# Performance work log

Measured on AMD Instinct MI355X. Metric: run time of the kernel, lower is better.

Reference implementation:

```python
import jax, jax.numpy as jnp
import numpy as np

NUM_EMB = 1024
EMB_DIM = 256
BETA = 0.25


def setup_inputs() -> dict:
    key = jax.random.key(0)
    k1, k2 = jax.random.split(key)
    z_e = jax.random.normal(k1, (32, EMB_DIM, 32, 32), dtype=jnp.float32)
    # original inits uniform(-1/num_emb, 1/num_emb)
    emb_weight = jax.random.uniform(k2, (NUM_EMB, EMB_DIM), dtype=jnp.float32,
                                    minval=-1.0 / NUM_EMB, maxval=1.0 / NUM_EMB)
    return {"z_e": z_e, "emb_weight": emb_weight}


def reference(z_e, emb_weight):
    # (B, C, H, W) -> (B, H, W, C)
    z = jnp.transpose(z_e, (0, 2, 3, 1))
    B, H, W, C = z.shape
    z_flat = z.reshape(-1, C)  # (N, C)
    # squared L2 distances to codebook: ||z||^2 + ||e||^2 - 2 z e^T
    d = (jnp.sum(z_flat ** 2, axis=1, keepdims=True)
         + jnp.sum(emb_weight ** 2, axis=1)
         - 2.0 * jnp.matmul(z_flat, emb_weight.T))  # (N, num_emb)
    encoding_indices = jnp.argmin(d, axis=1)  # (N,)
    # one-hot matmul == gather of codebook rows
    z_q = jnp.take(emb_weight, encoding_indices, axis=0).reshape(B, H, W, C)
    # vq losses
    L_e = jnp.mean((jax.lax.stop_gradient(z_q) - z) ** 2)
    L_q = jnp.mean((z_q - jax.lax.stop_gradient(z)) ** 2)
    vq_loss = L_e + BETA * L_q
    # straight-through estimator
    z_q_st = z + jax.lax.stop_gradient(z_q - z)
    z_q_out = jnp.transpose(z_q_st, (0, 3, 1, 2))  # (B, C, H, W)
    return z_q_out, vq_loss, encoding_indices
```

## Files before the change

### kernel.cpp

```cpp
#include <hip/hip_runtime.h>

#define NUM_EMB 1024
#define EMB_DIM 256
#define NPIX    32768
#define HW      1024
#define ZQ_ELEMS 8388608

#define WS_TNORM 8
#define WS_SNORM 8192
#define WS_KEYS  139264
#define WS_CNT   401408
#define WS_EPL   401424
#define EPLANE_ELEMS (NUM_EMB * EMB_DIM)

typedef unsigned long long u64;
typedef unsigned int u32;
typedef unsigned short u16;

typedef __bf16 bf16x8 __attribute__((ext_vector_type(8)));
typedef float f32x16 __attribute__((ext_vector_type(16)));
typedef u16 u16x8 __attribute__((ext_vector_type(8)));

#define ZIDX(row, q) (((row) << 5) + ((((q) ^ ((row) & 3))) << 3))

__device__ __forceinline__ float pw128_sq(const float* x, int stride) {
  float r[8];
#pragma unroll
  for (int j = 0; j < 8; ++j) {
    float v = x[(size_t)j * stride];
    r[j] = __fmul_rn(v, v);
  }
  for (int i = 8; i < 128; i += 8) {
#pragma unroll
    for (int j = 0; j < 8; ++j) {
      float v = x[(size_t)(i + j) * stride];
      r[j] = __fadd_rn(r[j], __fmul_rn(v, v));
    }
  }
  float s01 = __fadd_rn(r[0], r[1]);
  float s23 = __fadd_rn(r[2], r[3]);
  float s45 = __fadd_rn(r[4], r[5]);
  float s67 = __fadd_rn(r[6], r[7]);
  return __fadd_rn(__fadd_rn(s01, s23), __fadd_rn(s45, s67));
}

__device__ __forceinline__ void split3(float x, u16& h, u16& m, u16& l) {
  u32 u = __float_as_uint(x);
  u16 hb = (u16)((u + 0x7fffu + ((u >> 16) & 1u)) >> 16);
  float hf = __uint_as_float((u32)hb << 16);
  float r1 = x - hf;
  u32 u1 = __float_as_uint(r1);
  u16 mb = (u16)((u1 + 0x7fffu + ((u1 >> 16) & 1u)) >> 16);
  float mf = __uint_as_float((u32)mb << 16);
  float r2 = r1 - mf;
  u32 u2 = __float_as_uint(r2);
  u16 lb = (u16)((u2 + 0x7fffu + ((u2 >> 16) & 1u)) >> 16);
  h = hb; m = mb; l = lb;
}

__device__ __forceinline__ u64 shfl_xor_u64(u64 v, int msk) {
  const u32 lo = __shfl_xor((u32)v, msk, 64);
  const u32 hi = __shfl_xor((u32)(v >> 32), msk, 64);
  return ((u64)hi << 32) | lo;
}

__global__ __launch_bounds__(256) void vq_prep_kernel(
    const float* __restrict__ z, const float* __restrict__ emb,
    float* __restrict__ tnorm, float* __restrict__ snorm,
    unsigned long long* __restrict__ keys, double* __restrict__ loss_accum,
    u32* __restrict__ counter,
    u16* __restrict__ eh, u16* __restrict__ em, u16* __restrict__ el) {
  const int gid = blockIdx.x * 256 + threadIdx.x;
  if (gid == 0) *loss_accum = 0.0;
  if (gid == 1) *counter = 0u;
  if (gid < NPIX) {
    keys[gid] = ~0ull;
    const int b = gid >> 10, hw = gid & 1023;
    const float* base = z + (size_t)b * (EMB_DIM * HW) + hw;
    snorm[gid] = __fadd_rn(pw128_sq(base, HW), pw128_sq(base + (size_t)128 * HW, HW));
  } else {
    const int k = gid - NPIX;
    if (k < NUM_EMB) {
      const float* row = emb + (size_t)k * EMB_DIM;
      tnorm[k] = __fadd_rn(pw128_sq(row, 1), pw128_sq(row + 128, 1));
      for (int c = 0; c < EMB_DIM; c += 8) {
        u16x8 vh, vm, vl;
#pragma unroll
        for (int j = 0; j < 8; ++j) {
          u16 h_, m_, l_;
          split3(row[c + j], h_, m_, l_);
          vh[j] = h_; vm[j] = m_; vl[j] = l_;
        }
        *(u16x8*)(eh + (size_t)k * EMB_DIM + c) = vh;
        *(u16x8*)(em + (size_t)k * EMB_DIM + c) = vm;
        *(u16x8*)(el + (size_t)k * EMB_DIM + c) = vl;
      }
    }
  }
}

__global__ __launch_bounds__(256, 3) void vq_main_kernel(
    const float* __restrict__ z,
    const u16* __restrict__ eh, const u16* __restrict__ em,
    const u16* __restrict__ el,
    const float* __restrict__ tnorm, const float* __restrict__ snorm,
    unsigned long long* __restrict__ keys) {
  __shared__ __align__(16) u16 zs[3][4096];
  __shared__ __align__(16) u16 es[3][4096];

  const int t   = threadIdx.x;
  const int hb  = blockIdx.x;
  const int bid = (hb & 7) * 256 + (hb >> 3);
  const int pt  = bid >> 3;
  const int ntb = bid & 7;
  const int m0  = pt * 128;
  const int n0  = ntb * 128;
  const int b   = m0 >> 10;
  const int hw0 = m0 & 1023;
  const float* zbase = z + (size_t)b * (EMB_DIM * HW) + hw0;

  const int l    = t & 63;
  const int wid  = t >> 6;
  const int wpx0 = (wid >> 1) * 64;
  const int wcb  = (wid & 1) * 64;
  const int cl   = l & 31;
  const int hi   = l >> 5;

  const int sr  = t & 127;
  const int skh = (t >> 7) * 16;
  const int q0  = (t >> 7) * 2;

  const u16* eplan[3] = {eh, em, el};
  const size_t ebase = (size_t)(n0 + sr) * EMB_DIM + skh;

  float gz[16];
  u16x8 ge[3][2];

#pragma unroll
  for (int j = 0; j < 16; ++j)
    gz[j] = zbase[(size_t)(skh + j) * HW + sr];
#pragma unroll
  for (int p = 0; p < 3; ++p) {
    ge[p][0] = *(const u16x8*)(eplan[p] + ebase);
    ge[p][1] = *(const u16x8*)(eplan[p] + ebase + 8);
  }

  f32x16 acc[2][2];
#pragma unroll
  for (int i = 0; i < 2; ++i)
#pragma unroll
    for (int j = 0; j < 2; ++j)
#pragma unroll
      for (int r = 0; r < 16; ++r) acc[i][j][r] = 0.0f;

  for (int kt = 0; kt < 8; ++kt) {
#pragma unroll
    for (int c = 0; c < 2; ++c) {
      u16x8 vh, vm, vl;
#pragma unroll
      for (int j = 0; j < 8; ++j) {
        u16 h_, m_, l_;
        split3(gz[c * 8 + j], h_, m_, l_);
        vh[j] = h_; vm[j] = m_; vl[j] = l_;
      }
      const int zi = ZIDX(sr, q0 + c);
      *(u16x8*)&zs[0][zi] = vh;
      *(u16x8*)&zs[1][zi] = vm;
      *(u16x8*)&zs[2][zi] = vl;
    }
#pragma unroll
    for (int p = 0; p < 3; ++p) {
      *(u16x8*)&es[p][ZIDX(sr, q0)]     = ge[p][0];
      *(u16x8*)&es[p][ZIDX(sr, q0 + 1)] = ge[p][1];
    }
    if (kt < 7) {
      const int kb = (kt + 1) * 32;
#pragma unroll
      for (int j = 0; j < 16; ++j)
        gz[j] = zbase[(size_t)(kb + skh + j) * HW + sr];
#pragma unroll
      for (int p = 0; p < 3; ++p) {
        ge[p][0] = *(const u16x8*)(eplan[p] + ebase + kb);
        ge[p][1] = *(const u16x8*)(eplan[p] + ebase + kb + 8);
      }
    }
    __syncthreads();

#pragma unroll
    for (int ks = 0; ks < 2; ++ks) {
      const int q = ks * 2 + hi;
      bf16x8 af[3][2], bf[3][2];
#pragma unroll
      for (int p = 0; p < 3; ++p)
#pragma unroll
        for (int mt = 0; mt < 2; ++mt)
          af[p][mt] = *(const bf16x8*)&zs[p][ZIDX(wpx0 + mt * 32 + cl, q)];
#pragma unroll
      for (int p = 0; p < 3; ++p)
#pragma unroll
        for (int nn = 0; nn < 2; ++nn)
          bf[p][nn] = *(const bf16x8*)&es[p][ZIDX(wcb + nn * 32 + cl, q)];
#define PROD(PA, PB)                                                          \
      _Pragma("unroll")                                                       \
      for (int mt = 0; mt < 2; ++mt) {                                        \
        _Pragma("unroll")                                                     \
        for (int nn = 0; nn < 2; ++nn)                                        \
          acc[mt][nn] = __builtin_amdgcn_mfma_f32_32x32x16_bf16(              \
              af[PA][mt], bf[PB][nn], acc[mt][nn], 0, 0, 0);                  \
      }
      PROD(0, 0)
      PROD(0, 1)
      PROD(1, 0)
      PROD(1, 1)
      PROD(0, 2)
      PROD(2, 0)
#undef PROD
    }
    __syncthreads();
  }

  const float tv0 = tnorm[n0 + wcb + cl];
  const float tv1 = tnorm[n0 + wcb + 32 + cl];
  u64 bk[2][16];
#pragma unroll
  for (int mt = 0; mt < 2; ++mt)
#pragma unroll
    for (int reg = 0; reg < 16; ++reg) {
      const int row = wpx0 + mt * 32 + (reg & 3) + 8 * (reg >> 2) + 4 * hi;
      const float s = snorm[m0 + row];
      const float d0 = __fsub_rn(__fadd_rn(s, tv0), 2.0f * acc[mt][0][reg]);
      const float d1 = __fsub_rn(__fadd_rn(s, tv1), 2.0f * acc[mt][1][reg]);
      const u64 k0 = ((u64)__float_as_uint(d0) << 32) | (u32)(n0 + wcb + cl);
      const u64 k1 =
          ((u64)__float_as_uint(d1) << 32) | (u32)(n0 + wcb + 32 + cl);
      bk[mt][reg] = k0 < k1 ? k0 : k1;
    }
#pragma unroll
  for (int off = 1; off < 32; off <<= 1) {
#pragma unroll
    for (int mt = 0; mt < 2; ++mt)
#pragma unroll
      for (int reg = 0; reg < 16; ++reg) {
        const u64 o = shfl_xor_u64(bk[mt][reg], off);
        if (o < bk[mt][reg]) bk[mt][reg] = o;
      }
  }

  u64* part = (u64*)&zs[0][0];
  if (cl == 0) {
#pragma unroll
    for (int mt = 0; mt < 2; ++mt)
#pragma unroll
      for (int reg = 0; reg < 16; ++reg) {
        const int row = wpx0 + mt * 32 + (reg & 3) + 8 * (reg >> 2) + 4 * hi;
        part[row * 2 + (wid & 1)] = bk[mt][reg];
      }
  }
  __syncthreads();
  if (t < 128) {
    const u64 a = part[t * 2], c = part[t * 2 + 1];
    atomicMin(&keys[m0 + t], a < c ? a : c);
  }
}

__global__ __launch_bounds__(256) void vq_outputs_kernel(
    const float* __restrict__ z, const float* __restrict__ emb,
    const unsigned long long* __restrict__ keys, float* __restrict__ out,
    float* __restrict__ out_idx_f, double* __restrict__ loss_accum,
    u32* __restrict__ counter, float* __restrict__ out_loss) {
  const int t  = threadIdx.x;
  const int n0 = blockIdx.x * 64;
  const int m  = t & 63;
  const int c0 = t >> 6;
  const int b  = n0 >> 10;
  const int hw = n0 & 1023;
  const float* zb = z   + (size_t)b * (EMB_DIM * HW) + hw + m;
  float*       ob = out + (size_t)b * (EMB_DIM * HW) + hw + m;
  const int idx = (int)(u32)(keys[n0 + m] & 0xffffffffu);
  const float* er = emb + (size_t)idx * EMB_DIM;
  if (c0 == 0) out_idx_f[n0 + m] = (float)idx;

  double lsum = 0.0;
  for (int c = c0; c < EMB_DIM; c += 4) {
    const float e  = er[c];
    const float zv = zb[(size_t)c * HW];
    const float diff = e - zv;
    const float zq   = zv + diff;
    ob[(size_t)c * HW] = zq;
    lsum += (double)diff * (double)diff;
  }

  __shared__ double red[256];
  red[t] = lsum;
  __syncthreads();
  for (int s2 = 128; s2 > 0; s2 >>= 1) {
    if (t < s2) red[t] += red[t + s2];
    __syncthreads();
  }
  if (t == 0) {
    atomicAdd(loss_accum, red[0]);
    __threadfence();
    const u32 tick = atomicAdd(counter, 1u);
    if (tick == (u32)(NPIX / 64 - 1)) {
      const double total = atomicAdd(loss_accum, 0.0);
      const float L = (float)(total / (double)ZQ_ELEMS);
      out_loss[0] = __fadd_rn(L, __fmul_rn(0.25f, L));
    }
  }
}

extern "C" void kernel_launch(void* const* d_in, const int* in_sizes, int n_in,
                              void* d_out, int out_size, void* d_ws, size_t ws_size,
                              hipStream_t stream) {
  const float* z   = (const float*)d_in[0];
  const float* emb = (const float*)d_in[1];

  float* out       = (float*)d_out;
  float* out_loss  = out + ZQ_ELEMS;
  float* out_idx_f = out + ZQ_ELEMS + 1;

  double* loss_accum = (double*)d_ws;
  float*  tnorm = (float*)((char*)d_ws + WS_TNORM);
  float*  snorm = (float*)((char*)d_ws + WS_SNORM);
  unsigned long long* keys = (unsigned long long*)((char*)d_ws + WS_KEYS);
  u32* counter = (u32*)((char*)d_ws + WS_CNT);
  u16* eh = (u16*)((char*)d_ws + WS_EPL);
  u16* em = eh + EPLANE_ELEMS;
  u16* el = em + EPLANE_ELEMS;

  vq_prep_kernel<<<132, 256, 0, stream>>>(z, emb, tnorm, snorm, keys, loss_accum,
                                          counter, eh, em, el);
  vq_main_kernel<<<2048, 256, 0, stream>>>(z, eh, em, el, tnorm, snorm, keys);
  vq_outputs_kernel<<<NPIX / 64, 256, 0, stream>>>(z, emb, keys, out, out_idx_f,
                                                   loss_accum, counter, out_loss);
}
```

Baseline: 212.6 us.

## Replace XOR-swizzled LDS tiles with padded rows and coalesced codebook loads

Drops the XOR swizzle for the z and codebook shared-memory tiles and uses rows padded to 40 elements instead. Codebook tile loads are remapped so two threads cover each code row, which makes the global reads contiguous. Launch bounds drop from 3 to 2 blocks per CU, giving the compiler more registers but possibly lowering occupancy. The padded layout also uses more LDS per block.

```diff
diff --git a/kernel.cpp b/kernel.cpp
--- a/kernel.cpp
+++ b/kernel.cpp
@@ -20,8 +20,6 @@
 typedef __bf16 bf16x8 __attribute__((ext_vector_type(8)));
 typedef float f32x16 __attribute__((ext_vector_type(16)));
 typedef u16 u16x8 __attribute__((ext_vector_type(8)));
-
-#define ZIDX(row, q) (((row) << 5) + ((((q) ^ ((row) & 3))) << 3))
 
 __device__ __forceinline__ float pw128_sq(const float* x, int stride) {
   float r[8];
@@ -67,7 +65,7 @@
 __global__ __launch_bounds__(256) void vq_prep_kernel(
     const float* __restrict__ z, const float* __restrict__ emb,
     float* __restrict__ tnorm, float* __restrict__ snorm,
-    unsigned long long* __restrict__ keys, double* __restrict__ loss_accum,
+    u64* __restrict__ keys, double* __restrict__ loss_accum,
     u32* __restrict__ counter,
     u16* __restrict__ eh, u16* __restrict__ em, u16* __restrict__ el) {
   const int gid = blockIdx.x * 256 + threadIdx.x;
@@ -99,14 +97,14 @@
   }
 }
 
-__global__ __launch_bounds__(256, 3) void vq_main_kernel(
+__global__ __launch_bounds__(256, 2) void vq_main_kernel(
     const float* __restrict__ z,
     const u16* __restrict__ eh, const u16* __restrict__ em,
     const u16* __restrict__ el,
     const float* __restrict__ tnorm, const float* __restrict__ snorm,
-    unsigned long long* __restrict__ keys) {
-  __shared__ __align__(16) u16 zs[3][4096];
-  __shared__ __align__(16) u16 es[3][4096];
+    u64* __restrict__ keys) {
+  __shared__ __align__(16) u16 zs[3][128][40];
+  __shared__ __align__(16) u16 es[3][128][40];
 
   const int t   = threadIdx.x;
   const int hb  = blockIdx.x;
@@ -126,12 +124,12 @@
   const int cl   = l & 31;
   const int hi   = l >> 5;
 
-  const int sr  = t & 127;
-  const int skh = (t >> 7) * 16;
-  const int q0  = (t >> 7) * 2;
-
+  const int sr    = t & 127;
+  const int skh   = (t >> 7) * 16;
+  const int ecode = t >> 1;
+  const int ekh   = (t & 1) * 16;
   const u16* eplan[3] = {eh, em, el};
-  const size_t ebase = (size_t)(n0 + sr) * EMB_DIM + skh;
+  const size_t ebase = (size_t)(n0 + ecode) * EMB_DIM + ekh;
 
   float gz[16];
   u16x8 ge[3][2];
@@ -163,15 +161,14 @@
         split3(gz[c * 8 + j], h_, m_, l_);
         vh[j] = h_; vm[j] = m_; vl[j] = l_;
       }
-      const int zi = ZIDX(sr, q0 + c);
-      *(u16x8*)&zs[0][zi] = vh;
-      *(u16x8*)&zs[1][zi] = vm;
-      *(u16x8*)&zs[2][zi] = vl;
+      *(u16x8*)&zs[0][sr][skh + c * 8] = vh;
+      *(u16x8*)&zs[1][sr][skh + c * 8] = vm;
+      *(u16x8*)&zs[2][sr][skh + c * 8] = vl;
     }
 #pragma unroll
     for (int p = 0; p < 3; ++p) {
-      *(u16x8*)&es[p][ZIDX(sr, q0)]     = ge[p][0];
-      *(u16x8*)&es[p][ZIDX(sr, q0 + 1)] = ge[p][1];
+      *(u16x8*)&es[p][ecode][ekh]     = ge[p][0];
+      *(u16x8*)&es[p][ecode][ekh + 8] = ge[p][1];
     }
     if (kt < 7) {
       const int kb = (kt + 1) * 32;
@@ -188,18 +185,19 @@
 
 #pragma unroll
     for (int ks = 0; ks < 2; ++ks) {
-      const int q = ks * 2 + hi;
       bf16x8 af[3][2], bf[3][2];
 #pragma unroll
       for (int p = 0; p < 3; ++p)
 #pragma unroll
         for (int mt = 0; mt < 2; ++mt)
-          af[p][mt] = *(const bf16x8*)&zs[p][ZIDX(wpx0 + mt * 32 + cl, q)];
+          af[p][mt] =
+              *(const bf16x8*)&zs[p][wpx0 + mt * 32 + cl][ks * 16 + hi * 8];
 #pragma unroll
       for (int p = 0; p < 3; ++p)
 #pragma unroll
         for (int nn = 0; nn < 2; ++nn)
-          bf[p][nn] = *(const bf16x8*)&es[p][ZIDX(wcb + nn * 32 + cl, q)];
+          bf[p][nn] =
+              *(const bf16x8*)&es[p][wcb + nn * 32 + cl][ks * 16 + hi * 8];
 #define PROD(PA, PB)                                                          \
       _Pragma("unroll")                                                       \
       for (int mt = 0; mt < 2; ++mt) {                                        \
@@ -246,7 +244,7 @@
       }
   }
 
-  u64* part = (u64*)&zs[0][0];
+  u64* part = (u64*)&zs[0][0][0];
   if (cl == 0) {
 #pragma unroll
     for (int mt = 0; mt < 2; ++mt)
@@ -265,7 +263,7 @@
 
 __global__ __launch_bounds__(256) void vq_outputs_kernel(
     const float* __restrict__ z, const float* __restrict__ emb,
-    const unsigned long long* __restrict__ keys, float* __restrict__ out,
+    const u64* __restrict__ keys, float* __restrict__ out,
     float* __restrict__ out_idx_f, double* __restrict__ loss_accum,
     u32* __restrict__ counter, float* __restrict__ out_loss) {
   const int t  = threadIdx.x;
@@ -322,8 +320,8 @@
   double* loss_accum = (double*)d_ws;
   float*  tnorm = (float*)((char*)d_ws + WS_TNORM);
   float*  snorm = (float*)((char*)d_ws + WS_SNORM);
-  unsigned long long* keys = (unsigned long long*)((char*)d_ws + WS_KEYS);
-  u32* counter = (u32*)((char*)d_ws + WS_CNT);
+  u64*    keys  = (u64*)((char*)d_ws + WS_KEYS);
+  u32*    counter = (u32*)((char*)d_ws + WS_CNT);
   u16* eh = (u16*)((char*)d_ws + WS_EPL);
   u16* em = eh + EPLANE_ELEMS;
   u16* el = em + EPLANE_ELEMS;
```

Measured after the change: 204.1 us. 4.0% less time.
